# Optimization experiments

Hardware: AMD Instinct MI355X
Metric: run time of the kernel (lower is better)

## Reference

```python
import jax, jax.numpy as jnp
import numpy as np

B, L, D, H, FF = 2, 2048, 2048, 16, 8192
DH = D // H
NEG = -1e9


def setup_inputs() -> dict:
    key = jax.random.key(0)
    ks = jax.random.split(key, 9)
    x = jax.random.normal(ks[0], (B, L, D), dtype=jnp.float32)
    # additive causal mask, broadcastable to [B, H, L, L]
    causal = jnp.triu(jnp.full((L, L), NEG, dtype=jnp.float32), k=1)
    mask = causal[None, None, :, :]
    s = 1.0 / np.sqrt(D)
    Wq = jax.random.normal(ks[1], (D, D), dtype=jnp.float32) * s
    Wk = jax.random.normal(ks[2], (D, D), dtype=jnp.float32) * s
    Wv = jax.random.normal(ks[3], (D, D), dtype=jnp.float32) * s
    Wo = jax.random.normal(ks[4], (D, D), dtype=jnp.float32) * s
    W_up = jax.random.normal(ks[5], (FF, D), dtype=jnp.float32) * s
    b_up = jnp.zeros((FF,), dtype=jnp.float32)
    W_down = jax.random.normal(ks[6], (D, FF), dtype=jnp.float32) * (1.0 / np.sqrt(FF))
    return {"x": x, "mask": mask, "Wq": Wq, "Wk": Wk, "Wv": Wv, "Wo": Wo,
            "W_up": W_up, "b_up": b_up, "W_down": W_down}


def reference(x, mask, Wq, Wk, Wv, Wo, W_up, b_up, W_down):
    b, l, d = x.shape
    # projections (torch Linear: y = x @ W.T); reshape to [B, H, L, DH]
    q = (x @ Wq.T).reshape(b, l, H, DH).transpose(0, 2, 1, 3)
    k = (x @ Wk.T).reshape(b, l, H, DH).transpose(0, 2, 1, 3)
    v = (x @ Wv.T).reshape(b, l, H, DH).transpose(0, 2, 1, 3)
    # NOTE: original module applies NO 1/sqrt(d_head) scaling
    scores = jnp.einsum('bhqd,bhkd->bhqk', q, k) + mask
    attn = jax.nn.softmax(scores, axis=-1)
    out = jnp.einsum('bhqk,bhkd->bhqd', attn, v)
    out = out.transpose(0, 2, 1, 3).reshape(b, l, d)
    x = x + out @ Wo.T
    h = jax.nn.relu(x @ W_up.T + b_up)
    return x + h @ W_down.T
```

## Files before the change

kernel.cpp:

```cpp
#include <hip/hip_runtime.h>
#include <stdint.h>

typedef _Float16 f16;
typedef __attribute__((ext_vector_type(8))) _Float16 f16x8;
typedef __attribute__((ext_vector_type(4))) _Float16 f16x4;
typedef __attribute__((ext_vector_type(2))) __fp16 fp16x2;
typedef __attribute__((ext_vector_type(4))) float f32x4;
typedef __attribute__((ext_vector_type(16))) float f32x16;
typedef __attribute__((ext_vector_type(4))) unsigned u32x4;

__device__ __forceinline__ void gload16(void* lds, const void* gc) {
  void* g = const_cast<void*>(gc);
  __builtin_amdgcn_global_load_lds((__attribute__((address_space(1))) void*)g,
                                   (__attribute__((address_space(3))) void*)lds,
                                   16, 0, 0);
}

__device__ __forceinline__ unsigned pkrtz(float a, float b) {
  union { fp16x2 h; unsigned u; } c;
  c.h = __builtin_amdgcn_cvt_pkrtz(a, b);
  return c.u;
}

__global__ __launch_bounds__(256) void k_cast(const float* __restrict__ in,
                                              f16* __restrict__ out, int n4) {
  int stride = gridDim.x * blockDim.x;
  for (int i = blockIdx.x * blockDim.x + threadIdx.x; i < n4; i += stride) {
    float4 v = ((const float4*)in)[i];
    f16x4 o;
    o[0] = (f16)v.x; o[1] = (f16)v.y; o[2] = (f16)v.z; o[3] = (f16)v.w;
    ((f16x4*)out)[i] = o;
  }
}

__global__ __launch_bounds__(256) void k_cast4(const float* __restrict__ s0, const float* __restrict__ s1,
                                               const float* __restrict__ s2, const float* __restrict__ s3,
                                               f16* __restrict__ d0, f16* __restrict__ d1,
                                               f16* __restrict__ d2, f16* __restrict__ d3, int n4) {
  const int which = blockIdx.y;
  const float* in = which == 0 ? s0 : which == 1 ? s1 : which == 2 ? s2 : s3;
  f16* out = which == 0 ? d0 : which == 1 ? d1 : which == 2 ? d2 : d3;
  int stride = gridDim.x * blockDim.x;
  for (int i = blockIdx.x * blockDim.x + threadIdx.x; i < n4; i += stride) {
    float4 v = ((const float4*)in)[i];
    f16x4 o;
    o[0] = (f16)v.x; o[1] = (f16)v.y; o[2] = (f16)v.z; o[3] = (f16)v.w;
    ((f16x4*)out)[i] = o;
  }
}

__global__ __launch_bounds__(256) void k_cast2w(const float* __restrict__ s0, const float* __restrict__ s1,
                                                f16* __restrict__ d0, f16* __restrict__ d1, int n4) {
  const int which = blockIdx.y;
  const float* in = which == 0 ? s0 : s1;
  f16* out = which == 0 ? d0 : d1;
  int stride = gridDim.x * blockDim.x;
  for (int i = blockIdx.x * blockDim.x + threadIdx.x; i < n4; i += stride) {
    float4 v = ((const float4*)in)[i];
    f16x4 o;
    o[0] = (f16)v.x; o[1] = (f16)v.y; o[2] = (f16)v.z; o[3] = (f16)v.w;
    ((f16x4*)out)[i] = o;
  }
}

__global__ __launch_bounds__(256) void k_transpose_v(const f16* __restrict__ vp,
                                                     f16* __restrict__ vt) {
  __shared__ __attribute__((aligned(16))) f16 tile[64][66];
  const int lt = blockIdx.x, dt = blockIdx.y, bh = blockIdx.z;
  const int t = threadIdx.x;
  const int r = t >> 3, c = 8 * (t & 7);
  const f16* src = vp + ((size_t)bh * 2048 + lt * 64) * 128 + dt * 64;
#pragma unroll
  for (int i = 0; i < 2; ++i) {
    union { f16x8 v; unsigned u[4]; } uu;
    uu.v = *(const f16x8*)&src[(size_t)(i * 32 + r) * 128 + c];
#pragma unroll
    for (int j = 0; j < 4; ++j)
      *(unsigned*)&tile[i * 32 + r][c + 2 * j] = uu.u[j];
  }
  __syncthreads();
  f16* dst = vt + ((size_t)bh * 128 + dt * 64) * 2048 + lt * 64;
#pragma unroll
  for (int i = 0; i < 2; ++i) {
    const int dr = i * 32 + r;
    f16x8 o;
#pragma unroll
    for (int e = 0; e < 8; ++e) o[e] = tile[c + e][dr];
    *(f16x8*)&dst[(size_t)dr * 2048 + c] = o;
  }
}

__global__ __launch_bounds__(256) void k_fuseout(const f16* __restrict__ x1b,
                                                 const float* __restrict__ p0,
                                                 const float* __restrict__ p1,
                                                 float* __restrict__ out, int n4) {
  int stride = gridDim.x * blockDim.x;
  for (int i = blockIdx.x * blockDim.x + threadIdx.x; i < n4; i += stride) {
    float4 a = ((const float4*)p0)[i];
    float4 b = ((const float4*)p1)[i];
    f16x4 xb = ((const f16x4*)x1b)[i];
    float4 o;
    o.x = (float)xb[0] + a.x + b.x;
    o.y = (float)xb[1] + a.y + b.y;
    o.z = (float)xb[2] + a.z + b.z;
    o.w = (float)xb[3] + a.w + b.w;
    ((float4*)out)[i] = o;
  }
}

template <int EPI, int SPLITOUT, int BK>
__global__ __launch_bounds__(256, 4) void gemm_nt(const f16* __restrict__ A,
                                                  const f16* __restrict__ B,
                                                  int Kit, int ld, int N,
                                                  const float* __restrict__ res,
                                                  f16* __restrict__ outb) {
  constexpr int TSZ = 128 * BK;
  constexpr int CH  = 2048;
  constexpr int RPC = CH / BK;
  constexpr int NCH = 128 / RPC;
  constexpr int CW  = BK / 8;
  __shared__ __attribute__((aligned(16))) f16 As[TSZ];
  __shared__ __attribute__((aligned(16))) f16 Bs[TSZ];
  const int t = threadIdx.x;
  const int l = t & 63;
  const int w = t >> 6;
  const int wr = w >> 1, wc = w & 1;

  const int nwg = gridDim.x * gridDim.y;
  const int id = blockIdx.y * gridDim.x + blockIdx.x;
  const int sw = (id & 7) * (nwg >> 3) + (id >> 3);
  const int bn = sw % gridDim.x;
  const int bm = sw / gridDim.x;

  f32x4 acc[4][4] = {};

  const size_t aoff = (size_t)bm * 128 * ld;
  const size_t boff = (size_t)bn * 128 * ld;

  const int sr = t / CW;
  const int sc = 8 * (t % CW);
  const int lbase = w * 512;

  const int lr = l & 15, lq = l >> 4;
  const int nk = Kit / BK;
  for (int kt = 0; kt < nk; ++kt) {
    const size_t gbase = (size_t)kt * BK + (size_t)sr * ld + sc;
#pragma unroll
    for (int j = 0; j < NCH; ++j) {
      gload16(As + j * CH + lbase, A + aoff + (size_t)j * RPC * ld + gbase);
      gload16(Bs + j * CH + lbase, B + boff + (size_t)j * RPC * ld + gbase);
    }
    __syncthreads();
#pragma unroll
    for (int kk = 0; kk < BK / 32; ++kk) {
      f16x8 af[4], bfr[4];
#pragma unroll
      for (int m = 0; m < 4; ++m)
        af[m] = *(const f16x8*)&As[(wr * 64 + m * 16 + lr) * BK + kk * 32 + 8 * lq];
#pragma unroll
      for (int n = 0; n < 4; ++n)
        bfr[n] = *(const f16x8*)&Bs[(wc * 64 + n * 16 + lr) * BK + kk * 32 + 8 * lq];
#pragma unroll
      for (int m = 0; m < 4; ++m)
#pragma unroll
        for (int n = 0; n < 4; ++n)
          acc[m][n] = __builtin_amdgcn_mfma_f32_16x16x32_f16(af[m], bfr[n], acc[m][n], 0, 0, 0);
    }
    __syncthreads();
  }

#pragma unroll
  for (int m = 0; m < 4; ++m) {
#pragma unroll
    for (int r = 0; r < 4; ++r) {
      const int grow = bm * 128 + wr * 64 + m * 16 + lq * 4 + r;
#pragma unroll
      for (int n = 0; n < 4; ++n) {
        const int gcol = bn * 128 + wc * 64 + n * 16 + lr;
        const size_t idx = (size_t)grow * N + gcol;
        outb[idx] = (f16)(res[idx] + acc[m][n][r]);
      }
    }
  }
}

template <int EPI, int SPLITOUT>
__global__ __launch_bounds__(512, 4) void gemm8(const f16* __restrict__ A,
                                                const f16* __restrict__ B,
                                                int Kit, int ld, int N,
                                                const float* __restrict__ bias,
                                                float* __restrict__ outf,
                                                float* __restrict__ outf2,
                                                f16* __restrict__ outb,
                                                f16* __restrict__ outb_lo,
                                                f16* __restrict__ outv) {
  __shared__ __attribute__((aligned(16))) f16 As[3 * 4096];
  __shared__ __attribute__((aligned(16))) f16 Bs[3 * 8192];
  const int t = threadIdx.x;
  const int l = t & 63;
  const int w = t >> 6;
  const int wm = w >> 2, wn = w & 3;

  const int nwg = gridDim.x * gridDim.y;
  const int id = blockIdx.y * gridDim.x + blockIdx.x;
  const int sw = (id & 7) * (nwg >> 3) + (id >> 3);
  const int bn = sw % gridDim.x;
  const int bm = sw / gridDim.x;
  const int k0 = blockIdx.z * Kit;

  const size_t aoff = (size_t)(bm * 128) * ld + k0;
  const size_t boff = (size_t)(bn * 256) * ld + k0;

  const int r0 = t >> 2;
  const int gsw = (t & 3) ^ (r0 & 3) ^ ((r0 >> 2) & 3);
  const int ldsb = (t >> 6) * 512;

  auto stage = [&](int tt, int b) {
    const size_t col = (size_t)tt * 32 + gsw * 8;
    gload16(As + b * 4096 + ldsb, A + aoff + (size_t)r0 * ld + col);
#pragma unroll
    for (int j = 0; j < 2; ++j)
      gload16(Bs + b * 8192 + j * 4096 + ldsb, B + boff + (size_t)(j * 128 + r0) * ld + col);
  };

  f32x4 acc[4][4] = {};

  const int lr = l & 15, lq = l >> 4;
  const int xg = (lr & 3) ^ ((lr >> 2) & 3);
  const int nt = Kit >> 5;

  stage(0, 0);
  stage(1, 1);
  asm volatile("s_waitcnt vmcnt(3)" ::: "memory");
  __builtin_amdgcn_s_barrier();

  for (int kt = 0; kt < nt; ++kt) {
    const int b = kt % 3;
    const f16* Ab = As + b * 4096;
    const f16* Bb = Bs + b * 8192;
    f16x8 af[4], bf[4];
#pragma unroll
    for (int m = 0; m < 4; ++m)
      af[m] = *(const f16x8*)&Ab[(wm * 64 + m * 16 + lr) * 32 + ((lq ^ xg)) * 8];
#pragma unroll
    for (int n = 0; n < 4; ++n)
      bf[n] = *(const f16x8*)&Bb[(wn * 64 + n * 16 + lr) * 32 + ((lq ^ xg)) * 8];
    if (kt + 2 < nt) stage(kt + 2, (kt + 2) % 3);
    __builtin_amdgcn_s_setprio(1);
#pragma unroll
    for (int m = 0; m < 4; ++m)
#pragma unroll
      for (int n = 0; n < 4; ++n)
        acc[m][n] = __builtin_amdgcn_mfma_f32_16x16x32_f16(af[m], bf[n], acc[m][n], 0, 0, 0);
    __builtin_amdgcn_s_setprio(0);
    if (kt + 2 < nt) {
      asm volatile("s_waitcnt vmcnt(3)" ::: "memory");
    } else {
      asm volatile("s_waitcnt vmcnt(0)" ::: "memory");
    }
    __builtin_amdgcn_s_barrier();
  }

  const size_t QKS = (size_t)8 << 20;
#pragma unroll
  for (int m = 0; m < 4; ++m) {
#pragma unroll
    for (int r = 0; r < 4; ++r) {
      const int grow = bm * 128 + wm * 64 + m * 16 + lq * 4 + r;
#pragma unroll
      for (int n = 0; n < 4; ++n) {
        const int gcol = bn * 256 + wn * 64 + n * 16 + lr;
        const float v = acc[m][n][r];
        if constexpr (EPI == 0) {
          const int which = gcol >> 11;
          const int hcol = gcol & 2047;
          const int bb = grow >> 11, ll = grow & 2047;
          const int hh = hcol >> 7, dh = hcol & 127;
          const size_t idx = ((size_t)((bb * 16 + hh) * 2048 + ll) << 7) + dh;
          const f16 hv = (f16)v;
          if (which == 2) {
            outv[idx] = hv;
          } else {
            outb[which * QKS + idx] = hv;
            if constexpr (SPLITOUT) outb_lo[which * QKS + idx] = (f16)(v - (float)hv);
          }
        } else if constexpr (EPI == 2) {
          const size_t idx = (size_t)grow * N + gcol;
          outb[idx] = (f16)fmaxf(v + bias[gcol], 0.f);
        } else {
          const size_t idx = (size_t)grow * N + gcol;
          (blockIdx.z ? outf2 : outf)[idx] = v;
        }
      }
    }
  }
}

__global__ __launch_bounds__(256) void k_attn(const f16* __restrict__ q_hi,
                                              const f16* __restrict__ q_lo,
                                              const f16* __restrict__ k_hi,
                                              const f16* __restrict__ k_lo,
                                              const f16* __restrict__ vtp,
                                              f16* __restrict__ op) {
  __shared__ __attribute__((aligned(16))) f16 Ks_hi[64 * 128];
  __shared__ __attribute__((aligned(16))) f16 Ks_lo[64 * 128];
  __shared__ __attribute__((aligned(16))) f16 Vs[128 * 64];
  const int t = threadIdx.x, l = t & 63, w = t >> 6;
  const int flat = (int)blockIdx.x;
  const int s_ = flat >> 5;
  const int bh = flat & 31;
  const int qb = (s_ < 8) ? (15 - s_) : (s_ - 8);
  const int q0 = qb * 128;
  const int lh = l >> 5, lm = l & 31;
  const int wrow0 = q0 + 32 * w;
  const int myrow = wrow0 + lm;

  const f16* qhp = q_hi + (size_t)bh * 2048 * 128;
  const f16* qlp = q_lo + (size_t)bh * 2048 * 128;
  const f16* khp = k_hi + (size_t)bh * 2048 * 128;
  const f16* klp = k_lo + (size_t)bh * 2048 * 128;
  const f16* vhp = vtp + (size_t)bh * 128 * 2048;

  const int krow = t >> 4, kg = t & 15;
  const int vrow = t >> 3, vg = t & 7;

  f16x8 aqh[8], aql[8];
#pragma unroll
  for (int c = 0; c < 8; ++c) {
    const size_t qi = (size_t)myrow * 128 + c * 16 + 8 * lh;
    aqh[c] = *(const f16x8*)&qhp[qi];
    aql[c] = *(const f16x8*)&qlp[qi];
  }

  f32x16 acc[4] = {};
  float mr = -1e30f, sr = 0.f;

  const int ntile = 2 * qb + 2;
  for (int kt = 0; kt < ntile; ++kt) {
    f16x8 kh2[2], kl2[2], v2[2];
#pragma unroll
    for (int i = 0; i < 2; ++i) {
      const size_t ki = (size_t)(kt * 64 + i * 16 + krow) * 128 + 8 * kg;
      kh2[i] = *(const f16x8*)&khp[ki];
      kl2[i] = *(const f16x8*)&klp[ki];
      v2[i] = *(const f16x8*)&vhp[(size_t)(i * 32 + vrow) * 2048 + kt * 64 + 8 * vg];
    }
    __syncthreads();
#pragma unroll
    for (int i = 0; i < 2; ++i) {
      const int kr = i * 16 + krow;
      const int g = kg ^ (kr & 7);
      *(f16x8*)&Ks_hi[kr * 128 + 8 * g] = kh2[i];
      *(f16x8*)&Ks_lo[kr * 128 + 8 * g] = kl2[i];
      const int vr = i * 32 + vrow;
      const int gv = vg ^ (vr & 7);
      *(f16x8*)&Vs[vr * 64 + 8 * gv] = v2[i];
    }
#pragma unroll
    for (int i = 0; i < 2; ++i) {
      const size_t ki = (size_t)(kt * 64 + (i + 2) * 16 + krow) * 128 + 8 * kg;
      kh2[i] = *(const f16x8*)&khp[ki];
      kl2[i] = *(const f16x8*)&klp[ki];
      v2[i] = *(const f16x8*)&vhp[(size_t)((i + 2) * 32 + vrow) * 2048 + kt * 64 + 8 * vg];
    }
#pragma unroll
    for (int i = 0; i < 2; ++i) {
      const int kr = (i + 2) * 16 + krow;
      const int g = kg ^ (kr & 7);
      *(f16x8*)&Ks_hi[kr * 128 + 8 * g] = kh2[i];
      *(f16x8*)&Ks_lo[kr * 128 + 8 * g] = kl2[i];
      const int vr = (i + 2) * 32 + vrow;
      const int gv = vg ^ (vr & 7);
      *(f16x8*)&Vs[vr * 64 + 8 * gv] = v2[i];
    }
    __syncthreads();

    if (kt * 64 >= wrow0 + 32) continue;

    f32x16 s0, s1;
    __builtin_amdgcn_s_setprio(1);
    {
      f32x16 zh = {}, zl = {};
#pragma unroll
      for (int c = 0; c < 8; ++c) {
        const int g = (2 * c + lh) ^ (lm & 7);
        const f16x8 bh_ = *(const f16x8*)&Ks_hi[lm * 128 + 8 * g];
        const f16x8 bl_ = *(const f16x8*)&Ks_lo[lm * 128 + 8 * g];
        zh = __builtin_amdgcn_mfma_f32_32x32x16_f16(bh_, aqh[c], zh, 0, 0, 0);
        zl = __builtin_amdgcn_mfma_f32_32x32x16_f16(bh_, aql[c], zl, 0, 0, 0);
        zl = __builtin_amdgcn_mfma_f32_32x32x16_f16(bl_, aqh[c], zl, 0, 0, 0);
      }
      s0 = zh + zl;
    }
    {
      f32x16 zh = {}, zl = {};
#pragma unroll
      for (int c = 0; c < 8; ++c) {
        const int g = (2 * c + lh) ^ (lm & 7);
        const f16x8 bh_ = *(const f16x8*)&Ks_hi[(32 + lm) * 128 + 8 * g];
        const f16x8 bl_ = *(const f16x8*)&Ks_lo[(32 + lm) * 128 + 8 * g];
        zh = __builtin_amdgcn_mfma_f32_32x32x16_f16(bh_, aqh[c], zh, 0, 0, 0);
        zl = __builtin_amdgcn_mfma_f32_32x32x16_f16(bh_, aql[c], zl, 0, 0, 0);
        zl = __builtin_amdgcn_mfma_f32_32x32x16_f16(bl_, aqh[c], zl, 0, 0, 0);
      }
      s1 = zh + zl;
    }
    __builtin_amdgcn_s_setprio(0);

    if (kt * 64 + 63 > wrow0) {
#pragma unroll
      for (int j = 0; j < 16; ++j) {
        const int keyl = (j & 3) + 8 * (j >> 2) + 4 * lh;
        if (kt * 64 + keyl > myrow) s0[j] = -1e30f;
        if (kt * 64 + 32 + keyl > myrow) s1[j] = -1e30f;
      }
    }

    float m = -1e30f;
#pragma unroll
    for (int j = 0; j < 16; ++j) m = fmaxf(m, fmaxf(s0[j], s1[j]));
    m = fmaxf(m, __shfl_xor(m, 32));
    if (__any(m > mr + 8.f)) {
      const float mnew = fmaxf(mr, m);
      const float sc = __expf(mr - mnew);
      mr = mnew;
      sr *= sc;
#pragma unroll
      for (int j = 0; j < 16; ++j) {
        const float scj = __shfl(sc, (j & 3) + 8 * (j >> 2) + 4 * lh);
#pragma unroll
        for (int ct = 0; ct < 4; ++ct) acc[ct][j] *= scj;
      }
    }
    float p0v[16], p1v[16];
    float ts = 0.f;
#pragma unroll
    for (int j = 0; j < 16; ++j) {
      p0v[j] = __expf(s0[j] - mr);
      p1v[j] = __expf(s1[j] - mr);
      ts += p0v[j] + p1v[j];
    }
    sr += ts + __shfl_xor(ts, 32);

    unsigned u[16];
#pragma unroll
    for (int m2 = 0; m2 < 8; ++m2) {
      u[m2] = pkrtz(p0v[2 * m2], p0v[2 * m2 + 1]);
      u[8 + m2] = pkrtz(p1v[2 * m2], p1v[2 * m2 + 1]);
    }
    unsigned ys[8];
#pragma unroll
    for (int m2 = 0; m2 < 8; ++m2) {
      const int q_ = m2 >> 1, h_ = m2 & 1;
      const unsigned xs = lh ? u[4 * q_ + h_] : u[4 * q_ + 2 + h_];
      ys[m2] = __shfl_xor(xs, 32);
    }
    f16x8 pf[4];
#pragma unroll
    for (int kk = 0; kk < 4; ++kk) {
      union { u32x4 u4; f16x8 h8; } cv;
      if (lh == 0) {
        cv.u4[0] = u[4 * kk];     cv.u4[1] = u[4 * kk + 1];
        cv.u4[2] = ys[2 * kk];    cv.u4[3] = ys[2 * kk + 1];
      } else {
        cv.u4[0] = ys[2 * kk];    cv.u4[1] = ys[2 * kk + 1];
        cv.u4[2] = u[4 * kk + 2]; cv.u4[3] = u[4 * kk + 3];
      }
      pf[kk] = cv.h8;
    }

    __builtin_amdgcn_s_setprio(1);
#pragma unroll
    for (int ct = 0; ct < 4; ++ct) {
      const int dcol = ct * 32 + lm;
#pragma unroll
      for (int kk = 0; kk < 4; ++kk) {
        const int gv = (2 * kk + lh) ^ (dcol & 7);
        const f16x8 bv = *(const f16x8*)&Vs[dcol * 64 + 8 * gv];
        acc[ct] = __builtin_amdgcn_mfma_f32_32x32x16_f16(pf[kk], bv, acc[ct], 0, 0, 0);
      }
    }
    __builtin_amdgcn_s_setprio(0);
  }

  const int bb = bh >> 4, hh = bh & 15;
  const float inv = 1.f / sr;
#pragma unroll
  for (int j = 0; j < 16; ++j) {
    const int rl = (j & 3) + 8 * (j >> 2) + 4 * lh;
    const float invj = __shfl(inv, rl);
    const size_t row = (size_t)(bb * 2048 + wrow0 + rl);
#pragma unroll
    for (int ct = 0; ct < 4; ++ct)
      op[row * 2048 + hh * 128 + ct * 32 + lm] = (f16)(acc[ct][j] * invj);
  }
}

extern "C" void kernel_launch(void* const* d_in, const int* in_sizes, int n_in,
                              void* d_out, int out_size, void* d_ws, size_t ws_size,
                              hipStream_t stream) {
  const float* x   = (const float*)d_in[0];
  const float* Wq  = (const float*)d_in[2];
  const float* Wk  = (const float*)d_in[3];
  const float* Wv  = (const float*)d_in[4];
  const float* Wo  = (const float*)d_in[5];
  const float* Wup = (const float*)d_in[6];
  const float* bup = (const float*)d_in[7];
  const float* Wdn = (const float*)d_in[8];
  float* out = (float*)d_out;

  const size_t M1 = 1u << 20;
  f16* W = (f16*)d_ws;
  f16* x_hi    = W + 0 * M1;
  f16* wqkv_hi = W + 8 * M1;
  f16* wo_hi   = W + 20 * M1;
  f16* wup_hi  = W + 24 * M1;
  f16* wdn_hi  = W + 40 * M1;
  f16* q_hi    = W + 56 * M1;
  f16* q_lo    = W + 72 * M1;
  f16* vp      = W + 88 * M1;
  f16* vtb     = W + 96 * M1;
  f16* x1b   = x_hi;
  float* p0  = (float*)(W + 24 * M1);
  f16* hb    = W + 56 * M1;
  float* p1  = (float*)(W + 88 * M1);
  f16* attno = vp;
  if (ws_size < (size_t)104 * M1 * sizeof(f16)) return;

  auto cg = [](size_t n4) { size_t g = (n4 + 255) / 256; return (unsigned)(g > 2048 ? 2048 : g); };
  dim3 b256(256);
  dim3 b512(512);
  k_cast<<<cg(2 * M1), b256, 0, stream>>>(x, x_hi, (int)(2 * M1));
  k_cast4<<<dim3(cg(1 * M1), 4), b256, 0, stream>>>(
      Wq, Wk, Wv, Wo,
      wqkv_hi, wqkv_hi + 4 * M1, wqkv_hi + 8 * M1, wo_hi, (int)(1 * M1));
  k_cast2w<<<dim3(cg(4 * M1), 2), b256, 0, stream>>>(
      Wup, Wdn, wup_hi, wdn_hi, (int)(4 * M1));

  gemm8<0, 1><<<dim3(24, 32), b512, 0, stream>>>(
      x_hi, wqkv_hi, 2048, 2048, 6144,
      nullptr, nullptr, nullptr, q_hi, q_lo, vp);
  k_transpose_v<<<dim3(32, 2, 32), b256, 0, stream>>>(vp, vtb);
  k_attn<<<dim3(512), b256, 0, stream>>>(
      q_hi, q_lo, q_hi + 8 * M1, q_lo + 8 * M1, vtb, attno);
  gemm_nt<1, 0, 64><<<dim3(16, 32), b256, 0, stream>>>(
      attno, wo_hi, 2048, 2048, 2048, x, x1b);
  gemm8<2, 0><<<dim3(32, 32), b512, 0, stream>>>(
      x1b, wup_hi, 2048, 2048, 8192,
      bup, nullptr, nullptr, hb, nullptr, nullptr);
  gemm8<3, 0><<<dim3(8, 32, 2), b512, 0, stream>>>(
      hb, wdn_hi, 4096, 8192, 2048,
      nullptr, p0, p1, nullptr, nullptr, nullptr);
  k_fuseout<<<2048, b256, 0, stream>>>(x1b, p0, p1, out, (int)(2 * M1));
}
```

Measured before the change: 734.1 us.

## Replace 128x256 GEMM with 256x256 tile and phased half-tile LDS pipeline

The main f16 GEMM kernel moves from a 128x256 output tile with a 3-stage K=32 ring buffer to a 256x256 tile with K=64 double buffering. Each K tile is split into half-tile A/B loads that interleave with four MFMA phases, separated by barriers and lgkmcnt waits. The aim is more data reuse per LDS load and loads overlapped with compute for the QKV, up-projection and down-projection GEMMs. In exchange it uses more LDS (128KB) and twice the accumulators per wave, so occupancy drops. The grid halves in M, which may leave fewer workgroups than needed to fill the device.

```diff
diff --git a/kernel.cpp b/kernel.cpp
--- a/kernel.cpp
+++ b/kernel.cpp
@@ -185,17 +185,17 @@
 }
 
 template <int EPI, int SPLITOUT>
-__global__ __launch_bounds__(512, 4) void gemm8(const f16* __restrict__ A,
-                                                const f16* __restrict__ B,
-                                                int Kit, int ld, int N,
-                                                const float* __restrict__ bias,
-                                                float* __restrict__ outf,
-                                                float* __restrict__ outf2,
-                                                f16* __restrict__ outb,
-                                                f16* __restrict__ outb_lo,
-                                                f16* __restrict__ outv) {
-  __shared__ __attribute__((aligned(16))) f16 As[3 * 4096];
-  __shared__ __attribute__((aligned(16))) f16 Bs[3 * 8192];
+__global__ __launch_bounds__(512) void gemm9(const f16* __restrict__ A,
+                                             const f16* __restrict__ B,
+                                             int Kit, int ld, int N,
+                                             const float* __restrict__ bias,
+                                             float* __restrict__ outf,
+                                             float* __restrict__ outf2,
+                                             f16* __restrict__ outb,
+                                             f16* __restrict__ outb_lo,
+                                             f16* __restrict__ outv) {
+  __shared__ __attribute__((aligned(16))) f16 As[32768];
+  __shared__ __attribute__((aligned(16))) f16 Bs[32768];
   const int t = threadIdx.x;
   const int l = t & 63;
   const int w = t >> 6;
@@ -208,65 +208,120 @@
   const int bm = sw / gridDim.x;
   const int k0 = blockIdx.z * Kit;
 
-  const size_t aoff = (size_t)(bm * 128) * ld + k0;
+  const size_t aoff = (size_t)(bm * 256) * ld + k0;
   const size_t boff = (size_t)(bn * 256) * ld + k0;
 
-  const int r0 = t >> 2;
-  const int gsw = (t & 3) ^ (r0 & 3) ^ ((r0 >> 2) & 3);
+  const int r0a = t >> 3;
+  const int gsw = (t & 7) ^ (r0a & 7);
   const int ldsb = (t >> 6) * 512;
 
-  auto stage = [&](int tt, int b) {
-    const size_t col = (size_t)tt * 32 + gsw * 8;
-    gload16(As + b * 4096 + ldsb, A + aoff + (size_t)r0 * ld + col);
+  auto stageA = [&](int tile, int half) {
+    const size_t col = (size_t)tile * 64 + gsw * 8;
 #pragma unroll
     for (int j = 0; j < 2; ++j)
-      gload16(Bs + b * 8192 + j * 4096 + ldsb, B + boff + (size_t)(j * 128 + r0) * ld + col);
+      gload16(As + (tile & 1) * 16384 + half * 8192 + j * 4096 + ldsb,
+              A + aoff + (size_t)(half * 128 + j * 64 + r0a) * ld + col);
   };
-
-  f32x4 acc[4][4] = {};
+  auto stageB = [&](int tile, int half) {
+    const size_t col = (size_t)tile * 64 + gsw * 8;
+#pragma unroll
+    for (int j = 0; j < 2; ++j)
+      gload16(Bs + (tile & 1) * 16384 + half * 8192 + j * 4096 + ldsb,
+              B + boff + (size_t)(half * 128 + j * 64 + r0a) * ld + col);
+  };
+
+  f32x4 acc[8][4] = {};
+  f16x8 af[4][2], bf[4][2];
 
   const int lr = l & 15, lq = l >> 4;
-  const int xg = (lr & 3) ^ ((lr >> 2) & 3);
-  const int nt = Kit >> 5;
-
-  stage(0, 0);
-  stage(1, 1);
-  asm volatile("s_waitcnt vmcnt(3)" ::: "memory");
-  __builtin_amdgcn_s_barrier();
-
-  for (int kt = 0; kt < nt; ++kt) {
-    const int b = kt % 3;
-    const f16* Ab = As + b * 4096;
-    const f16* Bb = Bs + b * 8192;
-    f16x8 af[4], bf[4];
+
+  auto dsA = [&](int buf, int mh) {
+#pragma unroll
+    for (int m = 0; m < 4; ++m) {
+      const int row = mh * 64 + m * 16 + lr;
+#pragma unroll
+      for (int ks = 0; ks < 2; ++ks) {
+        const int g = (ks * 4 + lq) ^ (row & 7);
+        af[m][ks] = *(const f16x8*)&As[buf * 16384 + wm * 8192 + row * 64 + g * 8];
+      }
+    }
+  };
+  auto dsB = [&](int buf, int nh) {
+#pragma unroll
+    for (int n2 = 0; n2 < 2; ++n2) {
+      const int row = (wn & 1) * 64 + (nh * 2 + n2) * 16 + lr;
+#pragma unroll
+      for (int ks = 0; ks < 2; ++ks) {
+        const int g = (ks * 4 + lq) ^ (row & 7);
+        bf[nh * 2 + n2][ks] = *(const f16x8*)&Bs[buf * 16384 + (wn >> 1) * 8192 + row * 64 + g * 8];
+      }
+    }
+  };
+  auto mfma16 = [&](int mh, int nh) {
+    __builtin_amdgcn_s_setprio(1);
 #pragma unroll
     for (int m = 0; m < 4; ++m)
-      af[m] = *(const f16x8*)&Ab[(wm * 64 + m * 16 + lr) * 32 + ((lq ^ xg)) * 8];
-#pragma unroll
-    for (int n = 0; n < 4; ++n)
-      bf[n] = *(const f16x8*)&Bb[(wn * 64 + n * 16 + lr) * 32 + ((lq ^ xg)) * 8];
-    if (kt + 2 < nt) stage(kt + 2, (kt + 2) % 3);
-    __builtin_amdgcn_s_setprio(1);
-#pragma unroll
-    for (int m = 0; m < 4; ++m)
-#pragma unroll
-      for (int n = 0; n < 4; ++n)
-        acc[m][n] = __builtin_amdgcn_mfma_f32_16x16x32_f16(af[m], bf[n], acc[m][n], 0, 0, 0);
+#pragma unroll
+      for (int n2 = 0; n2 < 2; ++n2)
+#pragma unroll
+        for (int ks = 0; ks < 2; ++ks)
+          acc[mh * 4 + m][nh * 2 + n2] = __builtin_amdgcn_mfma_f32_16x16x32_f16(
+              af[m][ks], bf[nh * 2 + n2][ks], acc[mh * 4 + m][nh * 2 + n2], 0, 0, 0);
     __builtin_amdgcn_s_setprio(0);
-    if (kt + 2 < nt) {
-      asm volatile("s_waitcnt vmcnt(3)" ::: "memory");
-    } else {
-      asm volatile("s_waitcnt vmcnt(0)" ::: "memory");
-    }
-    __builtin_amdgcn_s_barrier();
-  }
+  };
+#define BAR() __builtin_amdgcn_s_barrier()
+#define LGKM() do { asm volatile("s_waitcnt lgkmcnt(0)" ::: "memory"); \
+                    __builtin_amdgcn_sched_barrier(0); } while (0)
+
+  const int ntk = Kit >> 6;
+  const int nj = ntk >> 1;
+
+  stageA(0, 0); stageA(0, 1); stageB(0, 0); stageB(0, 1);
+  stageB(1, 0); stageB(1, 1);
+  asm volatile("s_waitcnt vmcnt(4)" ::: "memory");
+  BAR();
+
+  for (int j = 0; j < nj; ++j) {
+    const int t1 = 2 * j + 1, t2 = 2 * j + 2, t3 = 2 * j + 3;
+    const bool last = (j == nj - 1);
+    dsA(0, 0); dsB(0, 0);
+    stageA(t1, 0);
+    BAR(); LGKM(); mfma16(0, 0); BAR();
+    dsB(0, 1);
+    stageA(t1, 1);
+    BAR(); LGKM(); mfma16(0, 1); BAR();
+    dsA(0, 1);
+    if (t2 < ntk) stageB(t2, 0);
+    BAR(); LGKM(); mfma16(1, 0); BAR();
+    if (t2 < ntk) stageB(t2, 1);
+    BAR(); mfma16(1, 1);
+    if (last) { asm volatile("s_waitcnt vmcnt(0)" ::: "memory"); }
+    else      { asm volatile("s_waitcnt vmcnt(4)" ::: "memory"); }
+    BAR();
+    dsA(1, 0); dsB(1, 0);
+    if (t2 < ntk) stageA(t2, 0);
+    BAR(); LGKM(); mfma16(0, 0); BAR();
+    dsB(1, 1);
+    if (t2 < ntk) stageA(t2, 1);
+    BAR(); LGKM(); mfma16(0, 1); BAR();
+    dsA(1, 1);
+    if (t3 < ntk) stageB(t3, 0);
+    BAR(); LGKM(); mfma16(1, 0); BAR();
+    if (t3 < ntk) stageB(t3, 1);
+    BAR(); mfma16(1, 1);
+    if (last) { asm volatile("s_waitcnt vmcnt(0)" ::: "memory"); }
+    else      { asm volatile("s_waitcnt vmcnt(4)" ::: "memory"); }
+    BAR();
+  }
+#undef BAR
+#undef LGKM
 
   const size_t QKS = (size_t)8 << 20;
 #pragma unroll
-  for (int m = 0; m < 4; ++m) {
+  for (int m = 0; m < 8; ++m) {
 #pragma unroll
     for (int r = 0; r < 4; ++r) {
-      const int grow = bm * 128 + wm * 64 + m * 16 + lq * 4 + r;
+      const int grow = bm * 256 + wm * 128 + m * 16 + lq * 4 + r;
 #pragma unroll
       for (int n = 0; n < 4; ++n) {
         const int gcol = bn * 256 + wn * 64 + n * 16 + lr;
@@ -537,7 +592,7 @@
   k_cast2w<<<dim3(cg(4 * M1), 2), b256, 0, stream>>>(
       Wup, Wdn, wup_hi, wdn_hi, (int)(4 * M1));
 
-  gemm8<0, 1><<<dim3(24, 32), b512, 0, stream>>>(
+  gemm9<0, 1><<<dim3(24, 16), b512, 0, stream>>>(
       x_hi, wqkv_hi, 2048, 2048, 6144,
       nullptr, nullptr, nullptr, q_hi, q_lo, vp);
   k_transpose_v<<<dim3(32, 2, 32), b256, 0, stream>>>(vp, vtb);
@@ -545,10 +600,10 @@
       q_hi, q_lo, q_hi + 8 * M1, q_lo + 8 * M1, vtb, attno);
   gemm_nt<1, 0, 64><<<dim3(16, 32), b256, 0, stream>>>(
       attno, wo_hi, 2048, 2048, 2048, x, x1b);
-  gemm8<2, 0><<<dim3(32, 32), b512, 0, stream>>>(
+  gemm9<2, 0><<<dim3(32, 16), b512, 0, stream>>>(
       x1b, wup_hi, 2048, 2048, 8192,
       bup, nullptr, nullptr, hb, nullptr, nullptr);
-  gemm8<3, 0><<<dim3(8, 32, 2), b512, 0, stream>>>(
+  gemm9<3, 0><<<dim3(8, 16, 2), b512, 0, stream>>>(
       hb, wdn_hi, 4096, 8192, 2048,
       nullptr, p0, p1, nullptr, nullptr, nullptr);
   k_fuseout<<<2048, b256, 0, stream>>>(x1b, p0, p1, out, (int)(2 * M1));
```

Result: faster. 693.8 us, median of 2 (-5.5%).
